# Kernel optimization log

Hardware: AMD Instinct MI355X
Metric: run time of the kernel (lower is better)

Reference implementation:

```python
import jax, jax.numpy as jnp
import numpy as np

NUM_HEADS = 8
ATTN_DIM = 512
DIM_HEAD = ATTN_DIM // NUM_HEADS
SCALE = DIM_HEAD ** -0.5
GN_EPS = 1e-5


def setup_inputs() -> dict:
    key = jax.random.key(0)
    k1, k2, k3 = jax.random.split(key, 3)
    B, H, W, C_IN, C_OUT = 8, 32, 32, 256, 256
    x = jax.random.normal(k1, (B, H, W, C_IN), dtype=jnp.float32)
    w_qkv = jax.random.normal(k2, (C_IN, 3 * ATTN_DIM), dtype=jnp.float32) * (C_IN ** -0.5)
    w_out = jax.random.normal(k3, (ATTN_DIM, C_OUT), dtype=jnp.float32) * (ATTN_DIM ** -0.5)
    b_out = jnp.zeros((C_OUT,), dtype=jnp.float32)
    gamma = jnp.ones((C_OUT,), dtype=jnp.float32)
    beta = jnp.zeros((C_OUT,), dtype=jnp.float32)
    return {"x": x, "w_qkv": w_qkv, "w_out": w_out, "b_out": b_out, "gamma": gamma, "beta": beta}


def reference(x, w_qkv, w_out, b_out, gamma, beta):
    B, H, W, _ = x.shape
    N = H * W
    # 1x1 conv QKV projection (no bias)
    qkv = jnp.einsum('bhwc,cd->bhwd', x, w_qkv)
    q, k, v = jnp.split(qkv, 3, axis=-1)
    # NHWC -> (B, heads, dim_head, HW), matching tf transpose+reshape
    def to_heads(t):
        return t.transpose(0, 3, 1, 2).reshape(B, NUM_HEADS, DIM_HEAD, N)
    q = to_heads(q) * SCALE
    k = to_heads(k)
    v = to_heads(v)
    # sim = q^T k over dim_head: (B, heads, N_q, N_k)
    sim = jnp.einsum('bhcn,bhcm->bhnm', q, k)
    attn = jax.nn.softmax(sim, axis=-1)  # includes the max-subtraction of the original
    # out = attn @ v^T: (B, heads, N, dim_head)
    out = jnp.einsum('bhnm,bhcm->bhnc', attn, v)
    # faithful tf.reshape((B,-1,H,W)) then NCHW->NHWC transpose
    out = out.reshape(B, -1, H, W).transpose(0, 2, 3, 1)  # (B, H, W, attn_dim)
    # output 1x1 conv (with bias) + GroupNorm(groups=1): normalize over (H, W, C) per sample
    y = jnp.einsum('bhwc,cd->bhwd', out, w_out) + b_out
    mean = jnp.mean(y, axis=(1, 2, 3), keepdims=True)
    var = jnp.var(y, axis=(1, 2, 3), keepdims=True)
    y = (y - mean) * jax.lax.rsqrt(var + GN_EPS)
    return y * gamma + beta
```

## Files before the change

kernel.cpp:

```cpp
#include <hip/hip_runtime.h>
#include <math.h>

#define NPOS   1024
#define CIN    256
#define DQKV   1536
#define ATTND  512
#define HEADS  8
#define DH     64
#define COUT   256
#define NBATCH 8
#define SCALE  0.125f
#define GN_EPS 1e-5f

typedef __attribute__((ext_vector_type(8))) __bf16 bf16x8;
typedef __attribute__((ext_vector_type(4))) __bf16 bf16x4;
typedef __attribute__((ext_vector_type(4))) float floatx4;
typedef __attribute__((ext_vector_type(8))) unsigned short ushort8;

#if __has_builtin(__builtin_amdgcn_exp2f)
#define EXP2(x) __builtin_amdgcn_exp2f(x)
#else
#define EXP2(x) exp2f(x)
#endif

#define GLOAD16(G, L) __builtin_amdgcn_global_load_lds( \
    (const __attribute__((address_space(1))) void*)(G), \
    (__attribute__((address_space(3))) void*)(L), 16, 0, 0)

#define OFF_WT   (4ull*1048576)
#define OFF_WOT  (4ull*1048576 + 786432ull)
#define OFF_QB   (5ull*1048576)
#define OFF_KB   (13ull*1048576)
#define OFF_VT   (29ull*1048576)
#define OFF_O2TT (45ull*1048576)
#define OFF_ST   (53ull*1048576)

__device__ inline ushort8 cvt_bf8(float4 a, float4 b) {
    bf16x8 o;
    o[0] = (__bf16)a.x; o[1] = (__bf16)a.y; o[2] = (__bf16)a.z; o[3] = (__bf16)a.w;
    o[4] = (__bf16)b.x; o[5] = (__bf16)b.y; o[6] = (__bf16)b.z; o[7] = (__bf16)b.w;
    return *(ushort8*)&o;
}

__global__ __launch_bounds__(256) void prep(
    const float* __restrict__ w_qkv, const float* __restrict__ w_out,
    unsigned short* __restrict__ wT, unsigned short* __restrict__ woT,
    float* __restrict__ stats)
{
    const int bid = blockIdx.x;
    const int t = threadIdx.x;
    __shared__ unsigned short tile[64][68];

    if (bid == 0) stats[t] = 0.0f;

    if (bid < 96) {
        const int n0 = (bid >> 2) * 64, k0 = (bid & 3) * 64;
        #pragma unroll
        for (int p = 0; p < 4; ++p) {
            const int row = p * 16 + (t >> 4);
            const int c = (t & 15) * 4;
            float4 a = *(const float4*)&w_qkv[(size_t)(k0 + row) * DQKV + n0 + c];
            float sv[4] = {a.x, a.y, a.z, a.w};
            #pragma unroll
            for (int j = 0; j < 4; ++j) {
                const float sc = (n0 + c + j) < 512 ? (SCALE * 1.44269504088896f) : 1.0f;
                __bf16 hb = (__bf16)(sv[j] * sc);
                tile[row][c + j] = *(unsigned short*)&hb;
            }
        }
        __syncthreads();
        const int nn = t >> 2;
        const int kc = (t & 3) * 16;
        unsigned short tmp[16];
        #pragma unroll
        for (int j = 0; j < 16; ++j) tmp[j] = tile[kc + j][nn];
        *(ushort8*)&wT[(size_t)(n0 + nn) * 256 + k0 + kc]     = *(ushort8*)&tmp[0];
        *(ushort8*)&wT[(size_t)(n0 + nn) * 256 + k0 + kc + 8] = *(ushort8*)&tmp[8];
        return;
    }

    const int idx = bid - 96;
    const int d0 = (idx & 3) * 64, k0 = (idx >> 2) * 64;
    #pragma unroll
    for (int p = 0; p < 4; ++p) {
        const int row = p * 16 + (t >> 4);
        const int c = (t & 15) * 4;
        float4 a = *(const float4*)&w_out[(size_t)(k0 + row) * COUT + d0 + c];
        float sv[4] = {a.x, a.y, a.z, a.w};
        #pragma unroll
        for (int j = 0; j < 4; ++j) {
            __bf16 hb = (__bf16)sv[j];
            tile[row][c + j] = *(unsigned short*)&hb;
        }
    }
    __syncthreads();
    {
        const int nn = t >> 2;
        const int kc = (t & 3) * 16;
        unsigned short tmp[16];
        #pragma unroll
        for (int j = 0; j < 16; ++j) tmp[j] = tile[kc + j][nn];
        *(ushort8*)&woT[(size_t)(d0 + nn) * 512 + k0 + kc]     = *(ushort8*)&tmp[0];
        *(ushort8*)&woT[(size_t)(d0 + nn) * 512 + k0 + kc + 8] = *(ushort8*)&tmp[8];
    }
}

__global__ __launch_bounds__(256) void qkv_gemm_mfma(
    const float* __restrict__ x, const __bf16* __restrict__ wT,
    __bf16* __restrict__ qb, __bf16* __restrict__ kb, __bf16* __restrict__ vT)
{
    const int t = threadIdx.x;
    const int w = t >> 6, lane = t & 63;
    const int col = lane & 15, qd = lane >> 4;
    const int wm = w >> 1, wn = w & 1;
    const int m0 = blockIdx.x * 128, n0 = blockIdx.y * 128;

    __shared__ __align__(16) unsigned short As[128][40];
    __shared__ __align__(16) unsigned short Bs[128][40];

    floatx4 zero4 = {0.f, 0.f, 0.f, 0.f};
    floatx4 acc[4][4];
    #pragma unroll
    for (int i = 0; i < 4; ++i)
        #pragma unroll
        for (int j = 0; j < 4; ++j) acc[i][j] = zero4;

    const int lrow = t >> 2, lc8 = (t & 3) * 8;

    float4 a0, a1, a2, a3;
    ushort8 breg[2];
    a0 = *(const float4*)&x[(size_t)(m0 + lrow) * 256 + lc8];
    a1 = *(const float4*)&x[(size_t)(m0 + lrow) * 256 + lc8 + 4];
    a2 = *(const float4*)&x[(size_t)(m0 + lrow + 64) * 256 + lc8];
    a3 = *(const float4*)&x[(size_t)(m0 + lrow + 64) * 256 + lc8 + 4];
    breg[0] = *(const ushort8*)&wT[(size_t)(n0 + lrow) * 256 + lc8];
    breg[1] = *(const ushort8*)&wT[(size_t)(n0 + lrow + 64) * 256 + lc8];

    for (int kk = 0; kk < 8; ++kk) {
        __syncthreads();
        *(ushort8*)&As[lrow][lc8]      = cvt_bf8(a0, a1);
        *(ushort8*)&As[lrow + 64][lc8] = cvt_bf8(a2, a3);
        *(ushort8*)&Bs[lrow][lc8]      = breg[0];
        *(ushort8*)&Bs[lrow + 64][lc8] = breg[1];
        __syncthreads();
        const int kn = (kk < 7) ? (kk + 1) * 32 : 0;
        a0 = *(const float4*)&x[(size_t)(m0 + lrow) * 256 + kn + lc8];
        a1 = *(const float4*)&x[(size_t)(m0 + lrow) * 256 + kn + lc8 + 4];
        a2 = *(const float4*)&x[(size_t)(m0 + lrow + 64) * 256 + kn + lc8];
        a3 = *(const float4*)&x[(size_t)(m0 + lrow + 64) * 256 + kn + lc8 + 4];
        breg[0] = *(const ushort8*)&wT[(size_t)(n0 + lrow) * 256 + kn + lc8];
        breg[1] = *(const ushort8*)&wT[(size_t)(n0 + lrow + 64) * 256 + kn + lc8];

        bf16x8 wf[4];
        #pragma unroll
        for (int ct = 0; ct < 4; ++ct)
            wf[ct] = *(const bf16x8*)&Bs[wn * 64 + ct * 16 + col][qd * 8];
        #pragma unroll
        for (int st = 0; st < 4; ++st) {
            bf16x8 xf = *(const bf16x8*)&As[wm * 64 + st * 16 + col][qd * 8];
            #pragma unroll
            for (int ct = 0; ct < 4; ++ct)
                acc[ct][st] = __builtin_amdgcn_mfma_f32_16x16x32_bf16(wf[ct], xf, acc[ct][st], 0, 0, 0);
        }
    }

    #pragma unroll
    for (int ct = 0; ct < 4; ++ct) {
        const int cbase = n0 + wn * 64 + ct * 16;
        const int sect = cbase >> 9;
        const int hh = (cbase >> 6) & 7;
        const int dd = (cbase & 63) + qd * 4;
        if (sect < 2) {
            __bf16* base = (sect == 0) ? qb : kb;
            #pragma unroll
            for (int st = 0; st < 4; ++st) {
                const int m = m0 + wm * 64 + st * 16 + col;
                const int b_ = m >> 10, n = m & 1023;
                bf16x4 o;
                #pragma unroll
                for (int r = 0; r < 4; ++r) o[r] = (__bf16)acc[ct][st][r];
                *(bf16x4*)&base[(((size_t)b_ * HEADS + hh) * NPOS + n) * DH + dd] = o;
            }
        } else {
            #pragma unroll
            for (int st = 0; st < 4; ++st) {
                const int m = m0 + wm * 64 + st * 16 + col;
                const int b_ = m >> 10, n = m & 1023;
                const size_t rowbase = ((size_t)(b_ * HEADS + hh) * DH + dd) * NPOS + n;
                #pragma unroll
                for (int r = 0; r < 4; ++r)
                    vT[rowbase + (size_t)r * NPOS] = (__bf16)acc[ct][st][r];
            }
        }
    }
}

__global__ __launch_bounds__(256, 2) void attn_mfma(
    const __bf16* __restrict__ qg, const __bf16* __restrict__ kg,
    const __bf16* __restrict__ vTg, __bf16* __restrict__ o2tT)
{
    const int bid = blockIdx.x;
    const int rid = (bid & 7) * 64 + (bid >> 3);
    const int qblk = rid & 7, h = (rid >> 3) & 7, b = rid >> 6;
    const int bh = b * HEADS + h;
    const int t = threadIdx.x;
    const int w = t >> 6, lane = t & 63;
    const int col = lane & 15;
    const int qd = lane >> 4;

    __shared__ __align__(16) unsigned short Kbuf[2][64][64];
    __shared__ __align__(16) unsigned short Vbuf[2][64][64];
    __shared__ __align__(16) unsigned short ps[4][32][68];

    bf16x8 qf0[2], qf1[2];
    #pragma unroll
    for (int s = 0; s < 2; ++s) {
        const __bf16* qptr = qg + ((size_t)bh * NPOS + qblk * 128 + s * 64 + w * 16 + col) * DH;
        qf0[s] = *(const bf16x8*)(qptr + qd * 8);
        qf1[s] = *(const bf16x8*)(qptr + 32 + qd * 8);
    }

    const char* kByte = (const char*)kg  + (size_t)bh * NPOS * DH * 2;
    const char* vByte = (const char*)vTg + (size_t)bh * DH * NPOS * 2;
    const int rsub = lane >> 3;
    const int csw  = ((lane & 7) * 16) ^ (rsub << 4);
    const char* ksrc0 = kByte + (size_t)(w * 8 + rsub) * 128  + csw;
    const char* vsrc0 = vByte + (size_t)(w * 8 + rsub) * 2048 + csw;

#define STAGE(B, KT) do {                                                    \
    const char* ks_ = ksrc0 + (size_t)(KT) * 8192;                           \
    const char* vs_ = vsrc0 + (size_t)(KT) * 128;                            \
    GLOAD16(ks_,         &Kbuf[B][0][0] + w * 512);                          \
    GLOAD16(ks_ + 4096,  &Kbuf[B][0][0] + 2048 + w * 512);                   \
    GLOAD16(vs_,         &Vbuf[B][0][0] + w * 512);                          \
    GLOAD16(vs_ + 65536, &Vbuf[B][0][0] + 2048 + w * 512);                   \
} while (0)

    floatx4 zero4 = {0.f, 0.f, 0.f, 0.f};
    floatx4 accO[2][4];
    #pragma unroll
    for (int s = 0; s < 2; ++s)
        #pragma unroll
        for (int i = 0; i < 4; ++i) accO[s][i] = zero4;
    floatx4 accL[2] = {zero4, zero4};
    bf16x8 ones8;
    #pragma unroll
    for (int j = 0; j < 8; ++j) ones8[j] = (__bf16)1.0f;

    const int swzc = (col & 7) << 4;
    const int offF0 = (qd * 16) ^ swzc;
    const int offF1 = (64 + qd * 16) ^ swzc;

    STAGE(0, 0);
    __syncthreads();

    int cur = 0;
    for (int kt = 0; kt < 16; ++kt) {
        if (kt < 15) STAGE(cur ^ 1, kt + 1);

        floatx4 accS[2][4];
        #pragma unroll
        for (int mt = 0; mt < 4; ++mt) {
            const char* krow = (const char*)&Kbuf[cur][mt * 16 + col][0];
            bf16x8 kf0 = *(const bf16x8*)(krow + offF0);
            bf16x8 kf1 = *(const bf16x8*)(krow + offF1);
            #pragma unroll
            for (int s = 0; s < 2; ++s) {
                accS[s][mt] = __builtin_amdgcn_mfma_f32_16x16x32_bf16(kf0, qf0[s], zero4, 0, 0, 0);
                accS[s][mt] = __builtin_amdgcn_mfma_f32_16x16x32_bf16(kf1, qf1[s], accS[s][mt], 0, 0, 0);
            }
        }

        #pragma unroll
        for (int s = 0; s < 2; ++s)
            #pragma unroll
            for (int mt = 0; mt < 4; ++mt) {
                bf16x4 pv;
                #pragma unroll
                for (int r = 0; r < 4; ++r) pv[r] = (__bf16)EXP2(accS[s][mt][r]);
                *(bf16x4*)&ps[w][s * 16 + col][mt * 16 + qd * 4] = pv;
            }

        bf16x8 pf0[2], pf1[2];
        #pragma unroll
        for (int s = 0; s < 2; ++s) {
            pf0[s] = *(const bf16x8*)&ps[w][s * 16 + col][qd * 8];
            pf1[s] = *(const bf16x8*)&ps[w][s * 16 + col][32 + qd * 8];
            accL[s] = __builtin_amdgcn_mfma_f32_16x16x32_bf16(ones8, pf0[s], accL[s], 0, 0, 0);
            accL[s] = __builtin_amdgcn_mfma_f32_16x16x32_bf16(ones8, pf1[s], accL[s], 0, 0, 0);
        }

        #pragma unroll
        for (int ct = 0; ct < 4; ++ct) {
            const char* vrow = (const char*)&Vbuf[cur][ct * 16 + col][0];
            bf16x8 vf0 = *(const bf16x8*)(vrow + offF0);
            bf16x8 vf1 = *(const bf16x8*)(vrow + offF1);
            #pragma unroll
            for (int s = 0; s < 2; ++s) {
                accO[s][ct] = __builtin_amdgcn_mfma_f32_16x16x32_bf16(vf0, pf0[s], accO[s][ct], 0, 0, 0);
                accO[s][ct] = __builtin_amdgcn_mfma_f32_16x16x32_bf16(vf1, pf1[s], accO[s][ct], 0, 0, 0);
            }
        }
        __syncthreads();
        cur ^= 1;
    }
#undef STAGE

    float inv_l[2];
    #pragma unroll
    for (int s = 0; s < 2; ++s) inv_l[s] = 1.0f / accL[s][0];

    unsigned short (*obuf)[8][68] = (unsigned short (*)[8][68])ps;
    __syncthreads();
    #pragma unroll
    for (int s = 0; s < 2; ++s)
        #pragma unroll
        for (int ct = 0; ct < 4; ++ct) {
            bf16x4 o;
            #pragma unroll
            for (int r = 0; r < 4; ++r) o[r] = (__bf16)(accO[s][ct][r] * inv_l[s]);
            *(bf16x4*)&obuf[col][s * 4 + w][ct * 16 + qd * 4] = o;
        }
    __syncthreads();
    const int chbase = h * 64 + qblk * 8;
    #pragma unroll
    for (int i = 0; i < 4; ++i) {
        const int p = i * 256 + t;
        const int pc = p >> 6, cc = p & 63;
        bf16x8 o;
        #pragma unroll
        for (int j = 0; j < 8; ++j) {
            unsigned short u = obuf[pc][j][cc];
            o[j] = *(__bf16*)&u;
        }
        *(bf16x8*)&o2tT[((size_t)b * NPOS + p) * ATTND + chbase] = o;
    }
}

__global__ __launch_bounds__(256) void out_mfma(
    const __bf16* __restrict__ a, const __bf16* __restrict__ woT,
    const float* __restrict__ b_out, float* __restrict__ y,
    float* __restrict__ stats)
{
    const int t = threadIdx.x;
    const int w = t >> 6, lane = t & 63;
    const int col = lane & 15, qd = lane >> 4;
    const int wm = w >> 1, wn = w & 1;
    const int m0 = blockIdx.x * 64, d0 = blockIdx.y * 64;
    const int b = blockIdx.x >> 4;

    __shared__ __align__(16) unsigned short As[64][72];
    __shared__ __align__(16) unsigned short Bs[64][72];
    __shared__ float reds[4], redq[4];

    floatx4 zero4 = {0.f, 0.f, 0.f, 0.f};
    floatx4 acc[2][2];
    #pragma unroll
    for (int i = 0; i < 2; ++i)
        #pragma unroll
        for (int j = 0; j < 2; ++j) acc[i][j] = zero4;

    const int lrow = t >> 2, lc = (t & 3) * 16;

    for (int k0 = 0; k0 < ATTND; k0 += 64) {
        __syncthreads();
        *(ushort8*)&As[lrow][lc]     = *(const ushort8*)&a[(size_t)(m0 + lrow) * ATTND + k0 + lc];
        *(ushort8*)&As[lrow][lc + 8] = *(const ushort8*)&a[(size_t)(m0 + lrow) * ATTND + k0 + lc + 8];
        *(ushort8*)&Bs[lrow][lc]     = *(const ushort8*)&woT[(size_t)(d0 + lrow) * ATTND + k0 + lc];
        *(ushort8*)&Bs[lrow][lc + 8] = *(const ushort8*)&woT[(size_t)(d0 + lrow) * ATTND + k0 + lc + 8];
        __syncthreads();
        bf16x8 af0[2], af1[2];
        #pragma unroll
        for (int mt = 0; mt < 2; ++mt) {
            af0[mt] = *(const bf16x8*)&As[wm * 32 + mt * 16 + col][qd * 8];
            af1[mt] = *(const bf16x8*)&As[wm * 32 + mt * 16 + col][32 + qd * 8];
        }
        #pragma unroll
        for (int nt = 0; nt < 2; ++nt) {
            bf16x8 bf0 = *(const bf16x8*)&Bs[wn * 32 + nt * 16 + col][qd * 8];
            bf16x8 bf1 = *(const bf16x8*)&Bs[wn * 32 + nt * 16 + col][32 + qd * 8];
            #pragma unroll
            for (int mt = 0; mt < 2; ++mt) {
                acc[mt][nt] = __builtin_amdgcn_mfma_f32_16x16x32_bf16(af0[mt], bf0, acc[mt][nt], 0, 0, 0);
                acc[mt][nt] = __builtin_amdgcn_mfma_f32_16x16x32_bf16(af1[mt], bf1, acc[mt][nt], 0, 0, 0);
            }
        }
    }

    float bias_n[2];
    #pragma unroll
    for (int nt = 0; nt < 2; ++nt) bias_n[nt] = b_out[d0 + wn * 32 + nt * 16 + col];

    float bsum = 0.0f, bsq = 0.0f;
    #pragma unroll
    for (int mt = 0; mt < 2; ++mt) {
        #pragma unroll
        for (int r = 0; r < 4; ++r) {
            const int m = m0 + wm * 32 + mt * 16 + qd * 4 + r;
            const int p = m & 1023;
            #pragma unroll
            for (int nt = 0; nt < 2; ++nt) {
                const int d = d0 + wn * 32 + nt * 16 + col;
                const float v = acc[mt][nt][r] + bias_n[nt];
                y[((size_t)b * NPOS + p) * COUT + d] = v;
                bsum += v;
                bsq  += v * v;
            }
        }
    }
    #pragma unroll
    for (int off = 1; off < 64; off <<= 1) {
        bsum += __shfl_xor(bsum, off);
        bsq  += __shfl_xor(bsq, off);
    }
    if (lane == 0) { reds[w] = bsum; redq[w] = bsq; }
    __syncthreads();
    if (t == 0) {
        atomicAdd(&stats[b * 16],       reds[0] + reds[1] + reds[2] + reds[3]);
        atomicAdd(&stats[128 + b * 16], redq[0] + redq[1] + redq[2] + redq[3]);
    }
}

__global__ __launch_bounds__(256) void gn_finalize(
    float* __restrict__ y, const float* __restrict__ stats,
    const float* __restrict__ gamma, const float* __restrict__ beta)
{
    const int idx = blockIdx.x * 256 + threadIdx.x;
    const int e = idx * 4;
    const int b_ = e >> 18;
    const int d = e & (COUT - 1);
    const float invn = 1.0f / (float)(NPOS * COUT);
    const float mean = stats[b_ * 16] * invn;
    const float var  = stats[128 + b_ * 16] * invn - mean * mean;
    const float rsig = rsqrtf(var + GN_EPS);
    float4 vv = *(float4*)&y[e];
    const float4 g  = *(const float4*)&gamma[d];
    const float4 bt = *(const float4*)&beta[d];
    vv.x = (vv.x - mean) * rsig * g.x + bt.x;
    vv.y = (vv.y - mean) * rsig * g.y + bt.y;
    vv.z = (vv.z - mean) * rsig * g.z + bt.z;
    vv.w = (vv.w - mean) * rsig * g.w + bt.w;
    *(float4*)&y[e] = vv;
}

extern "C" void kernel_launch(void* const* d_in, const int* in_sizes, int n_in,
                              void* d_out, int out_size, void* d_ws, size_t ws_size,
                              hipStream_t stream)
{
    const float* x     = (const float*)d_in[0];
    const float* w_qkv = (const float*)d_in[1];
    const float* w_out = (const float*)d_in[2];
    const float* b_out = (const float*)d_in[3];
    const float* gamma = (const float*)d_in[4];
    const float* beta  = (const float*)d_in[5];
    float* out = (float*)d_out;
    char* ws = (char*)d_ws;

    unsigned short* wT  = (unsigned short*)(ws + OFF_WT);
    unsigned short* woT = (unsigned short*)(ws + OFF_WOT);
    __bf16* qb  = (__bf16*)(ws + OFF_QB);
    __bf16* kb  = (__bf16*)(ws + OFF_KB);
    __bf16* vT  = (__bf16*)(ws + OFF_VT);
    __bf16* o2tT = (__bf16*)(ws + OFF_O2TT);
    float* stats = (float*)(ws + OFF_ST);

    prep         <<<dim3(128),    256, 0, stream>>>(w_qkv, w_out, wT, woT, stats);
    qkv_gemm_mfma<<<dim3(64, 12), 256, 0, stream>>>(x, (const __bf16*)wT, qb, kb, vT);
    attn_mfma    <<<dim3(512),    256, 0, stream>>>(qb, kb, vT, o2tT);
    out_mfma     <<<dim3(128, 4), 256, 0, stream>>>(o2tT, (const __bf16*)woT, b_out, out, stats);
    gn_finalize  <<<dim3(2048),   256, 0, stream>>>(out, stats, gamma, beta);
}
```

Baseline: 124.3 us.

## Pre-convert x to bf16, remap grids per XCD, shrink attention tiles, fuse GroupNorm

```diff
diff --git a/kernel.cpp b/kernel.cpp
--- a/kernel.cpp
+++ b/kernel.cpp
@@ -23,10 +23,7 @@
 #define EXP2(x) exp2f(x)
 #endif
 
-#define GLOAD16(G, L) __builtin_amdgcn_global_load_lds( \
-    (const __attribute__((address_space(1))) void*)(G), \
-    (__attribute__((address_space(3))) void*)(L), 16, 0, 0)
-
+#define OFF_XB   (0ull)
 #define OFF_WT   (4ull*1048576)
 #define OFF_WOT  (4ull*1048576 + 786432ull)
 #define OFF_QB   (5ull*1048576)
@@ -43,7 +40,9 @@
 }
 
 __global__ __launch_bounds__(256) void prep(
+    const float* __restrict__ x,
     const float* __restrict__ w_qkv, const float* __restrict__ w_out,
+    unsigned short* __restrict__ xb,
     unsigned short* __restrict__ wT, unsigned short* __restrict__ woT,
     float* __restrict__ stats)
 {
@@ -53,6 +52,18 @@
 
     if (bid == 0) stats[t] = 0.0f;
 
+    if (bid >= 128) {
+        const size_t base = (size_t)(bid - 128) * 8192 + (size_t)t * 8;
+        #pragma unroll
+        for (int i = 0; i < 4; ++i) {
+            const size_t off = base + (size_t)i * 2048;
+            const float4 u = *(const float4*)&x[off];
+            const float4 v = *(const float4*)&x[off + 4];
+            *(ushort8*)&xb[off] = cvt_bf8(u, v);
+        }
+        return;
+    }
+
     if (bid < 96) {
         const int n0 = (bid >> 2) * 64, k0 = (bid & 3) * 64;
         #pragma unroll
@@ -106,14 +117,18 @@
 }
 
 __global__ __launch_bounds__(256) void qkv_gemm_mfma(
-    const float* __restrict__ x, const __bf16* __restrict__ wT,
+    const unsigned short* __restrict__ xb, const __bf16* __restrict__ wT,
     __bf16* __restrict__ qb, __bf16* __restrict__ kb, __bf16* __restrict__ vT)
 {
+    const int bid = blockIdx.x;
+    const int xcd = bid & 7, local = bid >> 3;
+    const int m0 = (xcd * 8 + (local & 7)) * 128;
+    const int n0 = (local >> 3) * 128;
+
     const int t = threadIdx.x;
     const int w = t >> 6, lane = t & 63;
     const int col = lane & 15, qd = lane >> 4;
     const int wm = w >> 1, wn = w & 1;
-    const int m0 = blockIdx.x * 128, n0 = blockIdx.y * 128;
 
     __shared__ __align__(16) unsigned short As[128][40];
     __shared__ __align__(16) unsigned short Bs[128][40];
@@ -127,27 +142,22 @@
 
     const int lrow = t >> 2, lc8 = (t & 3) * 8;
 
-    float4 a0, a1, a2, a3;
-    ushort8 breg[2];
-    a0 = *(const float4*)&x[(size_t)(m0 + lrow) * 256 + lc8];
-    a1 = *(const float4*)&x[(size_t)(m0 + lrow) * 256 + lc8 + 4];
-    a2 = *(const float4*)&x[(size_t)(m0 + lrow + 64) * 256 + lc8];
-    a3 = *(const float4*)&x[(size_t)(m0 + lrow + 64) * 256 + lc8 + 4];
+    ushort8 areg[2], breg[2];
+    areg[0] = *(const ushort8*)&xb[(size_t)(m0 + lrow) * 256 + lc8];
+    areg[1] = *(const ushort8*)&xb[(size_t)(m0 + lrow + 64) * 256 + lc8];
     breg[0] = *(const ushort8*)&wT[(size_t)(n0 + lrow) * 256 + lc8];
     breg[1] = *(const ushort8*)&wT[(size_t)(n0 + lrow + 64) * 256 + lc8];
 
     for (int kk = 0; kk < 8; ++kk) {
         __syncthreads();
-        *(ushort8*)&As[lrow][lc8]      = cvt_bf8(a0, a1);
-        *(ushort8*)&As[lrow + 64][lc8] = cvt_bf8(a2, a3);
+        *(ushort8*)&As[lrow][lc8]      = areg[0];
+        *(ushort8*)&As[lrow + 64][lc8] = areg[1];
         *(ushort8*)&Bs[lrow][lc8]      = breg[0];
         *(ushort8*)&Bs[lrow + 64][lc8] = breg[1];
         __syncthreads();
         const int kn = (kk < 7) ? (kk + 1) * 32 : 0;
-        a0 = *(const float4*)&x[(size_t)(m0 + lrow) * 256 + kn + lc8];
-        a1 = *(const float4*)&x[(size_t)(m0 + lrow) * 256 + kn + lc8 + 4];
-        a2 = *(const float4*)&x[(size_t)(m0 + lrow + 64) * 256 + kn + lc8];
-        a3 = *(const float4*)&x[(size_t)(m0 + lrow + 64) * 256 + kn + lc8 + 4];
+        areg[0] = *(const ushort8*)&xb[(size_t)(m0 + lrow) * 256 + kn + lc8];
+        areg[1] = *(const ushort8*)&xb[(size_t)(m0 + lrow + 64) * 256 + kn + lc8];
         breg[0] = *(const ushort8*)&wT[(size_t)(n0 + lrow) * 256 + kn + lc8];
         breg[1] = *(const ushort8*)&wT[(size_t)(n0 + lrow + 64) * 256 + kn + lc8];
 
@@ -195,163 +205,149 @@
     }
 }
 
-__global__ __launch_bounds__(256, 2) void attn_mfma(
+__global__ __launch_bounds__(256, 4) void attn_mfma(
     const __bf16* __restrict__ qg, const __bf16* __restrict__ kg,
     const __bf16* __restrict__ vTg, __bf16* __restrict__ o2tT)
 {
     const int bid = blockIdx.x;
-    const int rid = (bid & 7) * 64 + (bid >> 3);
-    const int qblk = rid & 7, h = (rid >> 3) & 7, b = rid >> 6;
+    const int rid = (bid & 7) * 128 + (bid >> 3);
+    const int qblk = rid & 15, h = (rid >> 4) & 7, b = rid >> 7;
     const int bh = b * HEADS + h;
     const int t = threadIdx.x;
     const int w = t >> 6, lane = t & 63;
-    const int col = lane & 15;
-    const int qd = lane >> 4;
-
-    __shared__ __align__(16) unsigned short Kbuf[2][64][64];
-    __shared__ __align__(16) unsigned short Vbuf[2][64][64];
-    __shared__ __align__(16) unsigned short ps[4][32][68];
-
-    bf16x8 qf0[2], qf1[2];
-    #pragma unroll
-    for (int s = 0; s < 2; ++s) {
-        const __bf16* qptr = qg + ((size_t)bh * NPOS + qblk * 128 + s * 64 + w * 16 + col) * DH;
-        qf0[s] = *(const bf16x8*)(qptr + qd * 8);
-        qf1[s] = *(const bf16x8*)(qptr + 32 + qd * 8);
-    }
+    const int col = lane & 15, qd = lane >> 4;
+
+    __shared__ __align__(16) unsigned short Ks[64][64];
+    __shared__ __align__(16) unsigned short Vs[64][64];
+    __shared__ __align__(16) unsigned short ps[4][16][72];
+
+    const __bf16* qptr = qg + ((size_t)bh * NPOS + qblk * 64 + w * 16 + col) * DH;
+    bf16x8 qf0 = *(const bf16x8*)(qptr + qd * 8);
+    bf16x8 qf1 = *(const bf16x8*)(qptr + 32 + qd * 8);
 
     const char* kByte = (const char*)kg  + (size_t)bh * NPOS * DH * 2;
     const char* vByte = (const char*)vTg + (size_t)bh * DH * NPOS * 2;
-    const int rsub = lane >> 3;
-    const int csw  = ((lane & 7) * 16) ^ (rsub << 4);
-    const char* ksrc0 = kByte + (size_t)(w * 8 + rsub) * 128  + csw;
-    const char* vsrc0 = vByte + (size_t)(w * 8 + rsub) * 2048 + csw;
-
-#define STAGE(B, KT) do {                                                    \
-    const char* ks_ = ksrc0 + (size_t)(KT) * 8192;                           \
-    const char* vs_ = vsrc0 + (size_t)(KT) * 128;                            \
-    GLOAD16(ks_,         &Kbuf[B][0][0] + w * 512);                          \
-    GLOAD16(ks_ + 4096,  &Kbuf[B][0][0] + 2048 + w * 512);                   \
-    GLOAD16(vs_,         &Vbuf[B][0][0] + w * 512);                          \
-    GLOAD16(vs_ + 65536, &Vbuf[B][0][0] + 2048 + w * 512);                   \
-} while (0)
+
+    const int row0 = w * 16 + (lane >> 3);
+    const int seg  = lane & 7;
+    const char* ksrc = kByte + (size_t)row0 * 128  + seg * 16;
+    const char* vsrc = vByte + (size_t)row0 * 2048 + seg * 16;
+    const int swzo = (seg * 16) ^ ((row0 & 7) << 4);
+    unsigned short* kw0 = (unsigned short*)((char*)&Ks[row0][0] + swzo);
+    unsigned short* kw1 = (unsigned short*)((char*)&Ks[row0 + 8][0] + swzo);
+    unsigned short* vw0 = (unsigned short*)((char*)&Vs[row0][0] + swzo);
+    unsigned short* vw1 = (unsigned short*)((char*)&Vs[row0 + 8][0] + swzo);
+
+    ushort8 kreg[2], vreg[2];
+    kreg[0] = *(const ushort8*)(ksrc);
+    kreg[1] = *(const ushort8*)(ksrc + 1024);
+    vreg[0] = *(const ushort8*)(vsrc);
+    vreg[1] = *(const ushort8*)(vsrc + 16384);
 
     floatx4 zero4 = {0.f, 0.f, 0.f, 0.f};
-    floatx4 accO[2][4];
-    #pragma unroll
-    for (int s = 0; s < 2; ++s)
-        #pragma unroll
-        for (int i = 0; i < 4; ++i) accO[s][i] = zero4;
-    floatx4 accL[2] = {zero4, zero4};
+    floatx4 accO[4] = {zero4, zero4, zero4, zero4};
+    floatx4 accL = zero4;
     bf16x8 ones8;
     #pragma unroll
     for (int j = 0; j < 8; ++j) ones8[j] = (__bf16)1.0f;
 
-    const int swzc = (col & 7) << 4;
-    const int offF0 = (qd * 16) ^ swzc;
-    const int offF1 = (64 + qd * 16) ^ swzc;
-
-    STAGE(0, 0);
+    for (int kt = 0; kt < 16; ++kt) {
+        __syncthreads();
+        *(ushort8*)kw0 = kreg[0];
+        *(ushort8*)kw1 = kreg[1];
+        *(ushort8*)vw0 = vreg[0];
+        *(ushort8*)vw1 = vreg[1];
+        __syncthreads();
+        if (kt < 15) {
+            kreg[0] = *(const ushort8*)(ksrc + (size_t)(kt + 1) * 8192);
+            kreg[1] = *(const ushort8*)(ksrc + (size_t)(kt + 1) * 8192 + 1024);
+            vreg[0] = *(const ushort8*)(vsrc + (size_t)(kt + 1) * 128);
+            vreg[1] = *(const ushort8*)(vsrc + (size_t)(kt + 1) * 128 + 16384);
+        }
+
+        floatx4 accS[4];
+        #pragma unroll
+        for (int mt = 0; mt < 4; ++mt) {
+            const int kr = mt * 16 + col;
+            const char* krow = (const char*)&Ks[kr][0];
+            const int rsw = (kr & 7) << 4;
+            bf16x8 kf0 = *(const bf16x8*)(krow + ((qd * 16) ^ rsw));
+            bf16x8 kf1 = *(const bf16x8*)(krow + ((64 + qd * 16) ^ rsw));
+            accS[mt] = __builtin_amdgcn_mfma_f32_16x16x32_bf16(kf0, qf0, zero4, 0, 0, 0);
+            accS[mt] = __builtin_amdgcn_mfma_f32_16x16x32_bf16(kf1, qf1, accS[mt], 0, 0, 0);
+        }
+
+        #pragma unroll
+        for (int mt = 0; mt < 4; ++mt) {
+            bf16x4 pv;
+            #pragma unroll
+            for (int r = 0; r < 4; ++r) pv[r] = (__bf16)EXP2(accS[mt][r]);
+            *(bf16x4*)&ps[w][col][mt * 16 + qd * 4] = pv;
+        }
+
+        bf16x8 pf0 = *(const bf16x8*)&ps[w][col][qd * 8];
+        bf16x8 pf1 = *(const bf16x8*)&ps[w][col][32 + qd * 8];
+        accL = __builtin_amdgcn_mfma_f32_16x16x32_bf16(ones8, pf0, accL, 0, 0, 0);
+        accL = __builtin_amdgcn_mfma_f32_16x16x32_bf16(ones8, pf1, accL, 0, 0, 0);
+
+        #pragma unroll
+        for (int ct = 0; ct < 4; ++ct) {
+            const int vr = ct * 16 + col;
+            const char* vrow = (const char*)&Vs[vr][0];
+            const int rsw = (vr & 7) << 4;
+            bf16x8 vf0 = *(const bf16x8*)(vrow + ((qd * 16) ^ rsw));
+            bf16x8 vf1 = *(const bf16x8*)(vrow + ((64 + qd * 16) ^ rsw));
+            accO[ct] = __builtin_amdgcn_mfma_f32_16x16x32_bf16(vf0, pf0, accO[ct], 0, 0, 0);
+            accO[ct] = __builtin_amdgcn_mfma_f32_16x16x32_bf16(vf1, pf1, accO[ct], 0, 0, 0);
+        }
+    }
+
+    const float inv_l = 1.0f / accL[0];
+
+    #pragma unroll
+    for (int ct = 0; ct < 4; ++ct) {
+        bf16x4 o;
+        #pragma unroll
+        for (int r = 0; r < 4; ++r) o[r] = (__bf16)(accO[ct][r] * inv_l);
+        *(bf16x4*)&ps[w][col][ct * 16 + qd * 4] = o;
+    }
     __syncthreads();
-
-    int cur = 0;
-    for (int kt = 0; kt < 16; ++kt) {
-        if (kt < 15) STAGE(cur ^ 1, kt + 1);
-
-        floatx4 accS[2][4];
-        #pragma unroll
-        for (int mt = 0; mt < 4; ++mt) {
-            const char* krow = (const char*)&Kbuf[cur][mt * 16 + col][0];
-            bf16x8 kf0 = *(const bf16x8*)(krow + offF0);
-            bf16x8 kf1 = *(const bf16x8*)(krow + offF1);
-            #pragma unroll
-            for (int s = 0; s < 2; ++s) {
-                accS[s][mt] = __builtin_amdgcn_mfma_f32_16x16x32_bf16(kf0, qf0[s], zero4, 0, 0, 0);
-                accS[s][mt] = __builtin_amdgcn_mfma_f32_16x16x32_bf16(kf1, qf1[s], accS[s][mt], 0, 0, 0);
-            }
-        }
-
-        #pragma unroll
-        for (int s = 0; s < 2; ++s)
-            #pragma unroll
-            for (int mt = 0; mt < 4; ++mt) {
-                bf16x4 pv;
-                #pragma unroll
-                for (int r = 0; r < 4; ++r) pv[r] = (__bf16)EXP2(accS[s][mt][r]);
-                *(bf16x4*)&ps[w][s * 16 + col][mt * 16 + qd * 4] = pv;
-            }
-
-        bf16x8 pf0[2], pf1[2];
-        #pragma unroll
-        for (int s = 0; s < 2; ++s) {
-            pf0[s] = *(const bf16x8*)&ps[w][s * 16 + col][qd * 8];
-            pf1[s] = *(const bf16x8*)&ps[w][s * 16 + col][32 + qd * 8];
-            accL[s] = __builtin_amdgcn_mfma_f32_16x16x32_bf16(ones8, pf0[s], accL[s], 0, 0, 0);
-            accL[s] = __builtin_amdgcn_mfma_f32_16x16x32_bf16(ones8, pf1[s], accL[s], 0, 0, 0);
-        }
-
-        #pragma unroll
-        for (int ct = 0; ct < 4; ++ct) {
-            const char* vrow = (const char*)&Vbuf[cur][ct * 16 + col][0];
-            bf16x8 vf0 = *(const bf16x8*)(vrow + offF0);
-            bf16x8 vf1 = *(const bf16x8*)(vrow + offF1);
-            #pragma unroll
-            for (int s = 0; s < 2; ++s) {
-                accO[s][ct] = __builtin_amdgcn_mfma_f32_16x16x32_bf16(vf0, pf0[s], accO[s][ct], 0, 0, 0);
-                accO[s][ct] = __builtin_amdgcn_mfma_f32_16x16x32_bf16(vf1, pf1[s], accO[s][ct], 0, 0, 0);
-            }
-        }
-        __syncthreads();
-        cur ^= 1;
-    }
-#undef STAGE
-
-    float inv_l[2];
-    #pragma unroll
-    for (int s = 0; s < 2; ++s) inv_l[s] = 1.0f / accL[s][0];
-
-    unsigned short (*obuf)[8][68] = (unsigned short (*)[8][68])ps;
-    __syncthreads();
-    #pragma unroll
-    for (int s = 0; s < 2; ++s)
-        #pragma unroll
-        for (int ct = 0; ct < 4; ++ct) {
-            bf16x4 o;
-            #pragma unroll
-            for (int r = 0; r < 4; ++r) o[r] = (__bf16)(accO[s][ct][r] * inv_l[s]);
-            *(bf16x4*)&obuf[col][s * 4 + w][ct * 16 + qd * 4] = o;
-        }
-    __syncthreads();
-    const int chbase = h * 64 + qblk * 8;
+    const int cb = h * 64 + qblk * 4;
     #pragma unroll
     for (int i = 0; i < 4; ++i) {
         const int p = i * 256 + t;
-        const int pc = p >> 6, cc = p & 63;
-        bf16x8 o;
-        #pragma unroll
-        for (int j = 0; j < 8; ++j) {
-            unsigned short u = obuf[pc][j][cc];
+        const int qq = p >> 6, dd = p & 63;
+        bf16x4 o;
+        #pragma unroll
+        for (int j = 0; j < 4; ++j) {
+            unsigned short u = ps[j][qq][dd];
             o[j] = *(__bf16*)&u;
         }
-        *(bf16x8*)&o2tT[((size_t)b * NPOS + p) * ATTND + chbase] = o;
-    }
-}
-
-__global__ __launch_bounds__(256) void out_mfma(
+        *(bf16x4*)&o2tT[((size_t)b * NPOS + p) * ATTND + cb] = o;
+    }
+}
+
+__global__ __launch_bounds__(256, 2) void out_mfma(
     const __bf16* __restrict__ a, const __bf16* __restrict__ woT,
-    const float* __restrict__ b_out, float* __restrict__ y,
+    const float* __restrict__ b_out, const float* __restrict__ gamma,
+    const float* __restrict__ beta, float* __restrict__ y,
     float* __restrict__ stats)
 {
+    const int bid = blockIdx.x;
+    const int xcd = bid & 7, local = bid >> 3;
+    const int m0 = (xcd * 16 + (local & 15)) * 64;
+    const int d0 = (local >> 4) * 64;
+    const int b = xcd;
+
     const int t = threadIdx.x;
     const int w = t >> 6, lane = t & 63;
     const int col = lane & 15, qd = lane >> 4;
     const int wm = w >> 1, wn = w & 1;
-    const int m0 = blockIdx.x * 64, d0 = blockIdx.y * 64;
-    const int b = blockIdx.x >> 4;
 
     __shared__ __align__(16) unsigned short As[64][72];
     __shared__ __align__(16) unsigned short Bs[64][72];
     __shared__ float reds[4], redq[4];
+    __shared__ float sh_mean, sh_rsig;
 
     floatx4 zero4 = {0.f, 0.f, 0.f, 0.f};
     floatx4 acc[2][2];
@@ -387,11 +383,56 @@
         }
     }
 
-    float bias_n[2];
-    #pragma unroll
-    for (int nt = 0; nt < 2; ++nt) bias_n[nt] = b_out[d0 + wn * 32 + nt * 16 + col];
+    float bias_n[2], g_n[2], bt_n[2];
+    #pragma unroll
+    for (int nt = 0; nt < 2; ++nt) {
+        const int d = d0 + wn * 32 + nt * 16 + col;
+        bias_n[nt] = b_out[d];
+        g_n[nt]    = gamma[d];
+        bt_n[nt]   = beta[d];
+    }
 
     float bsum = 0.0f, bsq = 0.0f;
+    #pragma unroll
+    for (int mt = 0; mt < 2; ++mt)
+        #pragma unroll
+        for (int nt = 0; nt < 2; ++nt)
+            #pragma unroll
+            for (int r = 0; r < 4; ++r) {
+                const float v = acc[mt][nt][r] + bias_n[nt];
+                acc[mt][nt][r] = v;
+                bsum += v;
+                bsq  += v * v;
+            }
+    #pragma unroll
+    for (int off = 1; off < 64; off <<= 1) {
+        bsum += __shfl_xor(bsum, off);
+        bsq  += __shfl_xor(bsq, off);
+    }
+    if (lane == 0) { reds[w] = bsum; redq[w] = bsq; }
+    __syncthreads();
+
+    unsigned* cnt = (unsigned*)stats + 248;
+    if (t == 0) {
+        atomicAdd(&stats[b * 16],       reds[0] + reds[1] + reds[2] + reds[3]);
+        atomicAdd(&stats[128 + b * 16], redq[0] + redq[1] + redq[2] + redq[3]);
+        __threadfence();
+        atomicAdd(cnt, 1u);
+        int guard = 0;
+        while (__hip_atomic_load(cnt, __ATOMIC_ACQUIRE, __HIP_MEMORY_SCOPE_AGENT) < 512u) {
+            __builtin_amdgcn_s_sleep(8);
+            if (++guard > 2000000) break;
+        }
+        const float invn = 1.0f / (float)(NPOS * COUT);
+        const float mean = __hip_atomic_load(&stats[b * 16], __ATOMIC_RELAXED, __HIP_MEMORY_SCOPE_AGENT) * invn;
+        const float msq  = __hip_atomic_load(&stats[128 + b * 16], __ATOMIC_RELAXED, __HIP_MEMORY_SCOPE_AGENT) * invn;
+        sh_mean = mean;
+        sh_rsig = rsqrtf(msq - mean * mean + GN_EPS);
+    }
+    __syncthreads();
+
+    const float mean = sh_mean, rsig = sh_rsig;
+
     #pragma unroll
     for (int mt = 0; mt < 2; ++mt) {
         #pragma unroll
@@ -401,46 +442,11 @@
             #pragma unroll
             for (int nt = 0; nt < 2; ++nt) {
                 const int d = d0 + wn * 32 + nt * 16 + col;
-                const float v = acc[mt][nt][r] + bias_n[nt];
+                const float v = (acc[mt][nt][r] - mean) * rsig * g_n[nt] + bt_n[nt];
                 y[((size_t)b * NPOS + p) * COUT + d] = v;
-                bsum += v;
-                bsq  += v * v;
-            }
-        }
-    }
-    #pragma unroll
-    for (int off = 1; off < 64; off <<= 1) {
-        bsum += __shfl_xor(bsum, off);
-        bsq  += __shfl_xor(bsq, off);
-    }
-    if (lane == 0) { reds[w] = bsum; redq[w] = bsq; }
-    __syncthreads();
-    if (t == 0) {
-        atomicAdd(&stats[b * 16],       reds[0] + reds[1] + reds[2] + reds[3]);
-        atomicAdd(&stats[128 + b * 16], redq[0] + redq[1] + redq[2] + redq[3]);
-    }
-}
-
-__global__ __launch_bounds__(256) void gn_finalize(
-    float* __restrict__ y, const float* __restrict__ stats,
-    const float* __restrict__ gamma, const float* __restrict__ beta)
-{
-    const int idx = blockIdx.x * 256 + threadIdx.x;
-    const int e = idx * 4;
-    const int b_ = e >> 18;
-    const int d = e & (COUT - 1);
-    const float invn = 1.0f / (float)(NPOS * COUT);
-    const float mean = stats[b_ * 16] * invn;
-    const float var  = stats[128 + b_ * 16] * invn - mean * mean;
-    const float rsig = rsqrtf(var + GN_EPS);
-    float4 vv = *(float4*)&y[e];
-    const float4 g  = *(const float4*)&gamma[d];
-    const float4 bt = *(const float4*)&beta[d];
-    vv.x = (vv.x - mean) * rsig * g.x + bt.x;
-    vv.y = (vv.y - mean) * rsig * g.y + bt.y;
-    vv.z = (vv.z - mean) * rsig * g.z + bt.z;
-    vv.w = (vv.w - mean) * rsig * g.w + bt.w;
-    *(float4*)&y[e] = vv;
+            }
+        }
+    }
 }
 
 extern "C" void kernel_launch(void* const* d_in, const int* in_sizes, int n_in,
@@ -456,6 +462,7 @@
     float* out = (float*)d_out;
     char* ws = (char*)d_ws;
 
+    unsigned short* xb  = (unsigned short*)(ws + OFF_XB);
     unsigned short* wT  = (unsigned short*)(ws + OFF_WT);
     unsigned short* woT = (unsigned short*)(ws + OFF_WOT);
     __bf16* qb  = (__bf16*)(ws + OFF_QB);
@@ -464,9 +471,8 @@
     __bf16* o2tT = (__bf16*)(ws + OFF_O2TT);
     float* stats = (float*)(ws + OFF_ST);
 
-    prep         <<<dim3(128),    256, 0, stream>>>(w_qkv, w_out, wT, woT, stats);
-    qkv_gemm_mfma<<<dim3(64, 12), 256, 0, stream>>>(x, (const __bf16*)wT, qb, kb, vT);
-    attn_mfma    <<<dim3(512),    256, 0, stream>>>(qb, kb, vT, o2tT);
-    out_mfma     <<<dim3(128, 4), 256, 0, stream>>>(o2tT, (const __bf16*)woT, b_out, out, stats);
-    gn_finalize  <<<dim3(2048),   256, 0, stream>>>(out, stats, gamma, beta);
-}
+    prep         <<<dim3(384),  256, 0, stream>>>(x, w_qkv, w_out, xb, wT, woT, stats);
+    qkv_gemm_mfma<<<dim3(768),  256, 0, stream>>>(xb, (const __bf16*)wT, qb, kb, vT);
+    attn_mfma    <<<dim3(1024), 256, 0, stream>>>(qb, kb, vT, o2tT);
+    out_mfma     <<<dim3(512),  256, 0, stream>>>(o2tT, (const __bf16*)woT, b_out, gamma, beta, out, stats);
+}
```

After: 157.0 us. 1.26x slower.

## Pre-convert x to bf16, remap QKV GEMM blocks per XCD, raise attention occupancy

Applied to the files above, without the earlier changes.

```diff
diff --git a/kernel.cpp b/kernel.cpp
--- a/kernel.cpp
+++ b/kernel.cpp
@@ -27,6 +27,7 @@
     (const __attribute__((address_space(1))) void*)(G), \
     (__attribute__((address_space(3))) void*)(L), 16, 0, 0)
 
+#define OFF_XB   (0ull)
 #define OFF_WT   (4ull*1048576)
 #define OFF_WOT  (4ull*1048576 + 786432ull)
 #define OFF_QB   (5ull*1048576)
@@ -43,7 +44,9 @@
 }
 
 __global__ __launch_bounds__(256) void prep(
+    const float* __restrict__ x,
     const float* __restrict__ w_qkv, const float* __restrict__ w_out,
+    unsigned short* __restrict__ xb,
     unsigned short* __restrict__ wT, unsigned short* __restrict__ woT,
     float* __restrict__ stats)
 {
@@ -52,6 +55,18 @@
     __shared__ unsigned short tile[64][68];
 
     if (bid == 0) stats[t] = 0.0f;
+
+    if (bid >= 128) {
+        const size_t base = (size_t)(bid - 128) * 8192 + (size_t)t * 8;
+        #pragma unroll
+        for (int i = 0; i < 4; ++i) {
+            const size_t off = base + (size_t)i * 2048;
+            const float4 u = *(const float4*)&x[off];
+            const float4 v = *(const float4*)&x[off + 4];
+            *(ushort8*)&xb[off] = cvt_bf8(u, v);
+        }
+        return;
+    }
 
     if (bid < 96) {
         const int n0 = (bid >> 2) * 64, k0 = (bid & 3) * 64;
@@ -106,14 +121,18 @@
 }
 
 __global__ __launch_bounds__(256) void qkv_gemm_mfma(
-    const float* __restrict__ x, const __bf16* __restrict__ wT,
+    const unsigned short* __restrict__ xb, const __bf16* __restrict__ wT,
     __bf16* __restrict__ qb, __bf16* __restrict__ kb, __bf16* __restrict__ vT)
 {
+    const int bid = blockIdx.x;
+    const int xcd = bid & 7, local = bid >> 3;
+    const int m0 = (xcd * 8 + (local & 7)) * 128;
+    const int n0 = (local >> 3) * 128;
+
     const int t = threadIdx.x;
     const int w = t >> 6, lane = t & 63;
     const int col = lane & 15, qd = lane >> 4;
     const int wm = w >> 1, wn = w & 1;
-    const int m0 = blockIdx.x * 128, n0 = blockIdx.y * 128;
 
     __shared__ __align__(16) unsigned short As[128][40];
     __shared__ __align__(16) unsigned short Bs[128][40];
@@ -127,27 +146,22 @@
 
     const int lrow = t >> 2, lc8 = (t & 3) * 8;
 
-    float4 a0, a1, a2, a3;
-    ushort8 breg[2];
-    a0 = *(const float4*)&x[(size_t)(m0 + lrow) * 256 + lc8];
-    a1 = *(const float4*)&x[(size_t)(m0 + lrow) * 256 + lc8 + 4];
-    a2 = *(const float4*)&x[(size_t)(m0 + lrow + 64) * 256 + lc8];
-    a3 = *(const float4*)&x[(size_t)(m0 + lrow + 64) * 256 + lc8 + 4];
+    ushort8 areg[2], breg[2];
+    areg[0] = *(const ushort8*)&xb[(size_t)(m0 + lrow) * 256 + lc8];
+    areg[1] = *(const ushort8*)&xb[(size_t)(m0 + lrow + 64) * 256 + lc8];
     breg[0] = *(const ushort8*)&wT[(size_t)(n0 + lrow) * 256 + lc8];
     breg[1] = *(const ushort8*)&wT[(size_t)(n0 + lrow + 64) * 256 + lc8];
 
     for (int kk = 0; kk < 8; ++kk) {
         __syncthreads();
-        *(ushort8*)&As[lrow][lc8]      = cvt_bf8(a0, a1);
-        *(ushort8*)&As[lrow + 64][lc8] = cvt_bf8(a2, a3);
+        *(ushort8*)&As[lrow][lc8]      = areg[0];
+        *(ushort8*)&As[lrow + 64][lc8] = areg[1];
         *(ushort8*)&Bs[lrow][lc8]      = breg[0];
         *(ushort8*)&Bs[lrow + 64][lc8] = breg[1];
         __syncthreads();
         const int kn = (kk < 7) ? (kk + 1) * 32 : 0;
-        a0 = *(const float4*)&x[(size_t)(m0 + lrow) * 256 + kn + lc8];
-        a1 = *(const float4*)&x[(size_t)(m0 + lrow) * 256 + kn + lc8 + 4];
-        a2 = *(const float4*)&x[(size_t)(m0 + lrow + 64) * 256 + kn + lc8];
-        a3 = *(const float4*)&x[(size_t)(m0 + lrow + 64) * 256 + kn + lc8 + 4];
+        areg[0] = *(const ushort8*)&xb[(size_t)(m0 + lrow) * 256 + kn + lc8];
+        areg[1] = *(const ushort8*)&xb[(size_t)(m0 + lrow + 64) * 256 + kn + lc8];
         breg[0] = *(const ushort8*)&wT[(size_t)(n0 + lrow) * 256 + kn + lc8];
         breg[1] = *(const ushort8*)&wT[(size_t)(n0 + lrow + 64) * 256 + kn + lc8];
 
@@ -195,7 +209,7 @@
     }
 }
 
-__global__ __launch_bounds__(256, 2) void attn_mfma(
+__global__ __launch_bounds__(256, 3) void attn_mfma(
     const __bf16* __restrict__ qg, const __bf16* __restrict__ kg,
     const __bf16* __restrict__ vTg, __bf16* __restrict__ o2tT)
 {
@@ -258,6 +272,7 @@
     for (int kt = 0; kt < 16; ++kt) {
         if (kt < 15) STAGE(cur ^ 1, kt + 1);
 
+        __builtin_amdgcn_s_setprio(1);
         floatx4 accS[2][4];
         #pragma unroll
         for (int mt = 0; mt < 4; ++mt) {
@@ -301,6 +316,7 @@
                 accO[s][ct] = __builtin_amdgcn_mfma_f32_16x16x32_bf16(vf1, pf1[s], accO[s][ct], 0, 0, 0);
             }
         }
+        __builtin_amdgcn_s_setprio(0);
         __syncthreads();
         cur ^= 1;
     }
@@ -456,6 +472,7 @@
     float* out = (float*)d_out;
     char* ws = (char*)d_ws;
 
+    unsigned short* xb  = (unsigned short*)(ws + OFF_XB);
     unsigned short* wT  = (unsigned short*)(ws + OFF_WT);
     unsigned short* woT = (unsigned short*)(ws + OFF_WOT);
     __bf16* qb  = (__bf16*)(ws + OFF_QB);
@@ -464,9 +481,9 @@
     __bf16* o2tT = (__bf16*)(ws + OFF_O2TT);
     float* stats = (float*)(ws + OFF_ST);
 
-    prep         <<<dim3(128),    256, 0, stream>>>(w_qkv, w_out, wT, woT, stats);
-    qkv_gemm_mfma<<<dim3(64, 12), 256, 0, stream>>>(x, (const __bf16*)wT, qb, kb, vT);
-    attn_mfma    <<<dim3(512),    256, 0, stream>>>(qb, kb, vT, o2tT);
-    out_mfma     <<<dim3(128, 4), 256, 0, stream>>>(o2tT, (const __bf16*)woT, b_out, out, stats);
-    gn_finalize  <<<dim3(2048),   256, 0, stream>>>(out, stats, gamma, beta);
-}
+    prep         <<<dim3(384),     256, 0, stream>>>(x, w_qkv, w_out, xb, wT, woT, stats);
+    qkv_gemm_mfma<<<dim3(768),     256, 0, stream>>>(xb, (const __bf16*)wT, qb, kb, vT);
+    attn_mfma    <<<dim3(512),     256, 0, stream>>>(qb, kb, vT, o2tT);
+    out_mfma     <<<dim3(128, 4),  256, 0, stream>>>(o2tT, (const __bf16*)woT, b_out, out, stats);
+    gn_finalize  <<<dim3(2048),    256, 0, stream>>>(out, stats, gamma, beta);
+}
```

New measurement: 126.4 us. Within noise of the previous version (+1.8%).
